# Kernel tuning notes

Hardware: AMD Instinct MI355X
Metric: run time of the kernel (lower is better)

## Reference

```python
import jax, jax.numpy as jnp
import numpy as np

D = 768      # d_model (BERT-base)
H = 8        # MatTransformer heads
DK = D // H  # 96
L = 4        # MatTransformer layers
FF = 1024    # MatTransformer hidden_size
NREL = 97    # num_relations
BAG = 8      # bag_len (docs per bag)
SEQ = 512    # seq_len
NB = 3       # bridge entities per doc
S = 2 + NB   # spans per doc: h, t, bridges
E = BAG * S  # total entities = 40
NEG = -1e30


def setup_inputs() -> dict:
    key = jax.random.key(0)
    ks = jax.random.split(key, 30)
    w = lambda k, shp: jax.random.normal(k, shp, jnp.float32) * 0.02
    inp = {
        "embedding": jax.random.normal(ks[0], (BAG, SEQ, D), jnp.float32),
        "spans": jnp.sort(jax.random.randint(ks[1], (BAG, S, 2), 0, SEQ, jnp.int32), axis=-1),
        # Codred pairwise-relation params (torch Linear stored as [in, out])
        "wu_w": w(ks[2], (D, D)), "wu_b": jnp.zeros((D,), jnp.float32),
        "wvv_w": w(ks[3], (D, D)), "wvv_b": jnp.zeros((D,), jnp.float32),
        "lnr_w": w(ks[4], (D, D)), "lnr_b": jnp.zeros((D,), jnp.float32),
        # MatTransformer params, stacked over layers
        "matt_wq": w(ks[5], (L, D, D)), "matt_bq": jnp.zeros((L, D), jnp.float32),
        "matt_wk": w(ks[6], (L, D, D)), "matt_bk": jnp.zeros((L, D), jnp.float32),
        "matt_wv": w(ks[7], (L, D, D)), "matt_bv": jnp.zeros((L, D), jnp.float32),
        "matt_wo": w(ks[8], (L, D, D)), "matt_bo": jnp.zeros((L, D), jnp.float32),
        "matt_w1": w(ks[9], (L, D, FF)), "matt_b1": jnp.zeros((L, FF), jnp.float32),
        "matt_w2": w(ks[10], (L, FF, D)), "matt_b2": jnp.zeros((L, D), jnp.float32),
        "matt_g1": jnp.ones((L, D), jnp.float32), "matt_be1": jnp.zeros((L, D), jnp.float32),
        "matt_g2": jnp.ones((L, D), jnp.float32), "matt_be2": jnp.zeros((L, D), jnp.float32),
        # relation predictor
        "pred_w": w(ks[11], (D, NREL)), "pred_b": jnp.zeros((NREL,), jnp.float32),
    }
    return inp


def _layernorm(x, g, b, eps=1e-5):
    m = jnp.mean(x, axis=-1, keepdims=True)
    v = jnp.var(x, axis=-1, keepdims=True)
    return (x - m) * jax.lax.rsqrt(v + eps) * g + b


def reference(embedding, spans, wu_w, wu_b, wvv_w, wvv_b, lnr_w, lnr_b,
              matt_wq, matt_bq, matt_wk, matt_bk, matt_wv, matt_bv, matt_wo, matt_bo,
              matt_w1, matt_b1, matt_w2, matt_b2, matt_g1, matt_be1, matt_g2, matt_be2,
              pred_w, pred_b):
    # --- entity span max-pool (gather + max over inclusive [start, end]) ---
    pos = jnp.arange(SEQ)
    span_mask = (pos[None, None, :] >= spans[..., 0:1]) & (pos[None, None, :] <= spans[..., 1:2])  # [BAG,S,SEQ]
    pooled = jnp.max(jnp.where(span_mask[..., None], embedding[:, None, :, :], NEG), axis=2)  # [BAG,S,D]
    htb = pooled.reshape(E, D)  # per-doc order: h, t, b1..bNB (matches htb_embs stacking)

    # --- pairwise relation matrix: relu(ln1(relu(u_i + v_j))) ---
    u = htb @ wu_w + wu_b                       # [E,D]
    v = htb @ wvv_w + wvv_b                     # [E,D]
    alpha = jax.nn.relu(u[:, None, :] + v[None, :, :])          # [E,E,D]
    rel = jax.nn.relu(alpha @ lnr_w + lnr_b)                    # [E,E,D]

    # --- MatTransformer: encoder over the E*E relation tokens (rel_mask all ones) ---
    T = E * E
    x = rel.reshape(T, D)
    scale = 1.0 / np.sqrt(DK).astype(np.float32)
    for l in range(L):
        q = (x @ matt_wq[l] + matt_bq[l]).reshape(T, H, DK)
        k = (x @ matt_wk[l] + matt_bk[l]).reshape(T, H, DK)
        vv = (x @ matt_wv[l] + matt_bv[l]).reshape(T, H, DK)
        scores = jnp.einsum('thd,shd->hts', q, k) * scale       # [H,T,T]
        attn = jax.nn.softmax(scores, axis=-1)
        o = jnp.einsum('hts,shd->thd', attn, vv).reshape(T, D)
        o = o @ matt_wo[l] + matt_bo[l]
        x = _layernorm(x + o, matt_g1[l], matt_be1[l])
        ff = jax.nn.relu(x @ matt_w1[l] + matt_b1[l]) @ matt_w2[l] + matt_b2[l]
        x = _layernorm(x + ff, matt_g2[l], matt_be2[l])
    rel_m = x.reshape(E, E, D)

    # --- gather (h, t) relation features, predict, bag max-pool over logits ---
    h_pos = jnp.arange(BAG) * S      # head entity index per doc
    t_pos = h_pos + 1                # tail entity index per doc
    ht_feat = rel_m[h_pos, t_pos]    # [BAG,D]
    ht_logits = ht_feat @ pred_w + pred_b          # [BAG,NREL]
    bag_logit = jnp.max(ht_logits, axis=0, keepdims=True)  # [1,NREL]
    return bag_logit
```

## Files before the change

### kernel.cpp

```cpp
#include <hip/hip_runtime.h>


#define D    768
#define H    8
#define DKD  96
#define LAY  4
#define FFD  1024
#define NREL 97
#define BAG  8
#define SPANS 5
#define E    40
#define TT   1600
#define SEQ  512
#define D3   2304
#define NS   3
#define QT   (TT / 64)

typedef __attribute__((ext_vector_type(8))) short bf16x8;
typedef __attribute__((ext_vector_type(4))) float f32x4;
typedef unsigned short ushort_t;
typedef unsigned int uint_t;

__device__ __forceinline__ ushort_t f2b(float x) {
    uint_t u = __builtin_bit_cast(uint_t, x);
    return (ushort_t)((u + 0x7fffu + ((u >> 16) & 1u)) >> 16);
}
__device__ __forceinline__ float b2f(ushort_t v) {
    return __builtin_bit_cast(float, (uint_t)v << 16);
}

__device__ __forceinline__ void gload16(const void* g, void* l) {
    __builtin_amdgcn_global_load_lds(
        (const __attribute__((address_space(1))) unsigned int*)g,
        (__attribute__((address_space(3))) unsigned int*)l, 16, 0, 0);
}

__device__ __forceinline__ float block_sum(float v, float* red) {
#pragma unroll
    for (int o = 32; o >= 1; o >>= 1) v += __shfl_xor(v, o);
    __syncthreads();
    if ((threadIdx.x & 63) == 0) red[threadIdx.x >> 6] = v;
    __syncthreads();
    return red[0] + red[1] + red[2] + red[3];
}

__global__ __launch_bounds__(256) void span_pool_p1(const float* __restrict__ emb,
        const int* __restrict__ spans, float* __restrict__ partial) {
    const int e = blockIdx.x, pg = blockIdx.y;
    const int bag = e / SPANS;
    const int st = spans[e * 2 + 0];
    const int en = spans[e * 2 + 1];
    const int p0 = max(st, pg * 64);
    const int p1 = min(en, pg * 64 + 63);
    const int tid = threadIdx.x;
    if (tid >= 192) return;
    float4 m = make_float4(-1e30f, -1e30f, -1e30f, -1e30f);
    for (int p = p0; p <= p1; ++p) {
        const float4 v = *(const float4*)(emb + ((size_t)bag * SEQ + p) * D + tid * 4);
        m.x = fmaxf(m.x, v.x); m.y = fmaxf(m.y, v.y);
        m.z = fmaxf(m.z, v.z); m.w = fmaxf(m.w, v.w);
    }
    *(float4*)(partial + ((size_t)e * 8 + pg) * D + tid * 4) = m;
}

__global__ __launch_bounds__(256) void span_pool_p2(const float* __restrict__ partial,
        ushort_t* __restrict__ htb) {
    const int e = blockIdx.x;
    const int tid = threadIdx.x;
    if (tid >= 192) return;
    float4 m = make_float4(-1e30f, -1e30f, -1e30f, -1e30f);
#pragma unroll
    for (int pg = 0; pg < 8; ++pg) {
        const float4 v = *(const float4*)(partial + ((size_t)e * 8 + pg) * D + tid * 4);
        m.x = fmaxf(m.x, v.x); m.y = fmaxf(m.y, v.y);
        m.z = fmaxf(m.z, v.z); m.w = fmaxf(m.w, v.w);
    }
    ushort4 o;
    o.x = f2b(m.x); o.y = f2b(m.y); o.z = f2b(m.z); o.w = f2b(m.w);
    *(ushort4*)(htb + (size_t)e * D + tid * 4) = o;
}

__global__ __launch_bounds__(256) void alpha_k(const float* __restrict__ uv,
        ushort_t* __restrict__ a) {
    const int ij = blockIdx.x;
    const int i = ij / E, j = ij % E;
    const int tid = threadIdx.x;
#pragma unroll
    for (int t2 = 0; t2 < 3; ++t2) {
        const int d = tid + t2 * 256;
        a[(size_t)ij * D + d] =
            f2b(fmaxf(uv[(size_t)i * 1536 + d] + uv[(size_t)j * 1536 + 768 + d], 0.f));
    }
}

__global__ __launch_bounds__(256) void transpose_up(const float* __restrict__ lnr,
        const float* __restrict__ wu, const float* __restrict__ wvv,
        ushort_t* __restrict__ lnrT, ushort_t* __restrict__ wuvT) {
    __shared__ float t[32][33];
    const int z = blockIdx.z;
    const float* src = (z == 0) ? lnr : (z == 1) ? wu : wvv;
    ushort_t* dst = (z == 0) ? lnrT : wuvT + (size_t)(z - 1) * D * D;
    const int n0 = blockIdx.x * 32, k0 = blockIdx.y * 32;
    const int tx = threadIdx.x & 31, ty = threadIdx.x >> 5;
#pragma unroll
    for (int i = 0; i < 4; ++i)
        t[ty + i * 8][tx] = src[(size_t)(k0 + ty + i * 8) * D + n0 + tx];
    __syncthreads();
#pragma unroll
    for (int i = 0; i < 4; ++i)
        dst[(size_t)(n0 + ty + i * 8) * D + k0 + tx] = f2b(t[tx][ty + i * 8]);
}

__global__ __launch_bounds__(256) void transpose_layer(const float* __restrict__ wq,
        const float* __restrict__ wk, const float* __restrict__ wv,
        const float* __restrict__ wo, const float* __restrict__ w1,
        const float* __restrict__ w2, int l, ushort_t* __restrict__ wT4,
        ushort_t* __restrict__ w1T, ushort_t* __restrict__ w2T) {
    __shared__ float t[32][33];
    const int z = blockIdx.z;
    const float* src; ushort_t* dst; int K, N;
    if (z < 4) {
        K = D; N = D;
        src = (z == 0 ? wq : z == 1 ? wk : z == 2 ? wv : wo) + (size_t)l * D * D;
        dst = wT4 + (size_t)z * D * D;
    } else if (z == 4) {
        K = D; N = FFD; src = w1 + (size_t)l * D * FFD; dst = w1T;
    } else {
        K = FFD; N = D; src = w2 + (size_t)l * FFD * D; dst = w2T;
    }
    const int n0 = blockIdx.x * 32, k0 = blockIdx.y * 32;
    if (n0 >= N || k0 >= K) return;
    const int tx = threadIdx.x & 31, ty = threadIdx.x >> 5;
#pragma unroll
    for (int i = 0; i < 4; ++i)
        t[ty + i * 8][tx] = src[(size_t)(k0 + ty + i * 8) * N + n0 + tx];
    __syncthreads();
#pragma unroll
    for (int i = 0; i < 4; ++i)
        dst[(size_t)(n0 + ty + i * 8) * K + k0 + tx] = f2b(t[tx][ty + i * 8]);
}

__global__ __launch_bounds__(256) void concat_bias(const float* __restrict__ bq,
        const float* __restrict__ bk, const float* __restrict__ bv,
        const float* __restrict__ bu, const float* __restrict__ bvv,
        float* __restrict__ bqkv, float* __restrict__ buv) {
    const int i = blockIdx.x * 256 + threadIdx.x;
    if (i < LAY * D3) {
        const int l = i / D3, j = i % D3;
        bqkv[i] = j < D ? bq[l * D + j] : j < 2 * D ? bk[l * D + j - D] : bv[l * D + j - 2 * D];
    }
    const int k = i - LAY * D3;
    if (k >= 0 && k < 2 * D) buv[k] = k < D ? bu[k] : bvv[k - D];
}

template<int RELU, int SCALEQ, int SPLITK, int HEADMAJ>
__global__ __launch_bounds__(256) void gemm_mfma(const ushort_t* __restrict__ A,
        const ushort_t* __restrict__ Bt, const float* __restrict__ bias,
        float* __restrict__ Cf, float* __restrict__ Cf1,
        ushort_t* __restrict__ Cb, int M, int N, int K) {
    __shared__ ushort_t As[2][128 * 32];
    __shared__ ushort_t Bs[2][64 * 32];
    const int tid = threadIdx.x;
    const int lane = tid & 63, w = tid >> 6;
    const int l15 = lane & 15, lg = lane >> 4;
    const int bm = blockIdx.y * 128, bn = blockIdx.x * 64;
    const int wm = (w >> 1) * 64, wn = (w & 1) * 32;
    const int trA0 = w * 32 + (lane >> 2);
    const int trA1 = trA0 + 16;
    const int trB  = w * 16 + (lane >> 2);
    const int sc   = (lane & 3) * 8;
    const size_t rowA0 = (size_t)min(bm + trA0, M - 1) * K;
    const size_t rowA1 = (size_t)min(bm + trA1, M - 1) * K;
    const size_t rowB  = (size_t)(bn + trB) * K;
    const int kbeg = SPLITK ? blockIdx.z * (K / 2) : 0;
    const int kend = SPLITK ? kbeg + K / 2 : K;

    f32x4 acc[4][2];
#pragma unroll
    for (int mi = 0; mi < 4; ++mi)
#pragma unroll
        for (int ni = 0; ni < 2; ++ni)
            acc[mi][ni] = (f32x4){0.f, 0.f, 0.f, 0.f};

    auto STAGE = [&](int buf, int k0) {
        gload16(A + rowA0 + k0 + sc, As[buf] + w * 1024);
        gload16(A + rowA1 + k0 + sc, As[buf] + w * 1024 + 512);
        gload16(Bt + rowB + k0 + sc, Bs[buf] + w * 512);
    };

    const int ntk = (kend - kbeg) / 32;
    STAGE(0, kbeg);
    __syncthreads();
    for (int t = 0; t < ntk; ++t) {
        const int buf = t & 1;
        if (t + 1 < ntk) STAGE(buf ^ 1, kbeg + (t + 1) * 32);
        bf16x8 af[4], bfr[2];
#pragma unroll
        for (int mi = 0; mi < 4; ++mi)
            af[mi] = *(const bf16x8*)&As[buf][(wm + mi * 16 + l15) * 32 + lg * 8];
#pragma unroll
        for (int ni = 0; ni < 2; ++ni)
            bfr[ni] = *(const bf16x8*)&Bs[buf][(wn + ni * 16 + l15) * 32 + lg * 8];
        __builtin_amdgcn_s_setprio(1);
#pragma unroll
        for (int mi = 0; mi < 4; ++mi)
#pragma unroll
            for (int ni = 0; ni < 2; ++ni)
                acc[mi][ni] = __builtin_amdgcn_mfma_f32_16x16x32_bf16(
                    af[mi], bfr[ni], acc[mi][ni], 0, 0, 0);
        __builtin_amdgcn_s_setprio(0);
        __syncthreads();
    }
    float* Cout = (SPLITK && blockIdx.z) ? Cf1 : Cf;
    const bool addb = !(SPLITK && blockIdx.z);
#pragma unroll
    for (int mi = 0; mi < 4; ++mi)
#pragma unroll
        for (int ni = 0; ni < 2; ++ni)
#pragma unroll
            for (int r = 0; r < 4; ++r) {
                const int row = bm + wm + mi * 16 + lg * 4 + r;
                if (row >= M) continue;
                const int col = bn + wn + ni * 16 + l15;
                float v = acc[mi][ni][r] + (addb ? bias[col] : 0.f);
                if (RELU) v = fmaxf(v, 0.f);
                if (SCALEQ) { if (col < D) v *= 0.10206207261596577f; }
                if (Cout) Cout[(size_t)row * N + col] = v;
                if (Cb) {
                    if (HEADMAJ) {
                        const int m = col / D;
                        const int rem = col - m * D;
                        const int hd = rem / DKD;
                        const int dd = rem - hd * DKD;
                        Cb[(((size_t)m * H + hd) * TT + row) * DKD + dd] = f2b(v);
                    } else {
                        Cb[(size_t)row * N + col] = f2b(v);
                    }
                }
            }
}

__global__ __launch_bounds__(256) void attn_part(const ushort_t* __restrict__ kvh,
        ushort_t* __restrict__ Opart, float* __restrict__ ml) {
    __shared__ ushort_t Ks[64][104];
    __shared__ ushort_t Vt[96][72];
    __shared__ ushort_t Ps[4][16][72];
    const int q0 = blockIdx.x * 64;
    const int h = blockIdx.y;
    const int cch = blockIdx.z;
    const int t_lo = (cch * QT) / NS;
    const int t_hi = ((cch + 1) * QT) / NS;
    const int tid = threadIdx.x;
    const int lane = tid & 63, w = tid >> 6;
    const int l15 = lane & 15, lg = lane >> 4;

    const ushort_t* Qb = kvh + (size_t)h * TT * DKD;
    const ushort_t* Kb = kvh + ((size_t)H + h) * TT * DKD;
    const ushort_t* Vb = kvh + ((size_t)2 * H + h) * TT * DKD;

    int r_[3], c_[3];
#pragma unroll
    for (int i = 0; i < 3; ++i) {
        const int ch = i * 256 + tid;
        r_[i] = ch / 12; c_[i] = (ch % 12) * 8;
    }
    bf16x8 qfrag[3];
#pragma unroll
    for (int ks = 0; ks < 3; ++ks)
        qfrag[ks] = *(const bf16x8*)(Qb + (size_t)(q0 + w * 16 + l15) * DKD
                                     + ks * 32 + lg * 8);
    uint4 kreg[3], vreg[3];
    {
        const int s0 = t_lo * 64;
#pragma unroll
        for (int i = 0; i < 3; ++i) {
            kreg[i] = *(const uint4*)(Kb + (size_t)(s0 + r_[i]) * DKD + c_[i]);
            vreg[i] = *(const uint4*)(Vb + (size_t)(s0 + r_[i]) * DKD + c_[i]);
        }
    }
    float m_run[4], l_run[4];
    f32x4 acc_o[6];
#pragma unroll
    for (int r = 0; r < 4; ++r) { m_run[r] = -1e30f; l_run[r] = 0.f; }
#pragma unroll
    for (int nt = 0; nt < 6; ++nt) acc_o[nt] = (f32x4){0.f, 0.f, 0.f, 0.f};

    for (int t = t_lo; t < t_hi; ++t) {
        __syncthreads();
#pragma unroll
        for (int i = 0; i < 3; ++i) {
            *(uint4*)&Ks[r_[i]][c_[i]] = kreg[i];
            const ushort_t* pv = (const ushort_t*)&vreg[i];
            const int kk = r_[i] ^ (((c_[i] >> 3) & 7) << 3);
#pragma unroll
            for (int j = 0; j < 8; ++j) Vt[c_[i] + j][kk] = pv[j];
        }
        __syncthreads();
        if (t + 1 < t_hi) {
            const int s0 = (t + 1) * 64;
#pragma unroll
            for (int i = 0; i < 3; ++i) {
                kreg[i] = *(const uint4*)(Kb + (size_t)(s0 + r_[i]) * DKD + c_[i]);
                vreg[i] = *(const uint4*)(Vb + (size_t)(s0 + r_[i]) * DKD + c_[i]);
            }
        }
        f32x4 accs[4];
#pragma unroll
        for (int ni = 0; ni < 4; ++ni) accs[ni] = (f32x4){0.f, 0.f, 0.f, 0.f};
        __builtin_amdgcn_s_setprio(1);
#pragma unroll
        for (int ks = 0; ks < 3; ++ks) {
#pragma unroll
            for (int ni = 0; ni < 4; ++ni) {
                const bf16x8 bk = *(const bf16x8*)&Ks[ni * 16 + l15][ks * 32 + lg * 8];
                accs[ni] = __builtin_amdgcn_mfma_f32_16x16x32_bf16(qfrag[ks], bk, accs[ni], 0, 0, 0);
            }
        }
        __builtin_amdgcn_s_setprio(0);
        float mx[4];
#pragma unroll
        for (int r = 0; r < 4; ++r) {
            mx[r] = fmaxf(fmaxf(accs[0][r], accs[1][r]), fmaxf(accs[2][r], accs[3][r]));
#pragma unroll
            for (int o = 1; o <= 8; o <<= 1) mx[r] = fmaxf(mx[r], __shfl_xor(mx[r], o));
        }
        const bool grow = (mx[0] > m_run[0] + 8.f) || (mx[1] > m_run[1] + 8.f) ||
                          (mx[2] > m_run[2] + 8.f) || (mx[3] > m_run[3] + 8.f);
        if (__any(grow)) {
#pragma unroll
            for (int r = 0; r < 4; ++r) {
                const float mnew = fmaxf(m_run[r], mx[r]);
                const float sf = __expf(m_run[r] - mnew);
                m_run[r] = mnew;
                l_run[r] *= sf;
#pragma unroll
                for (int nt = 0; nt < 6; ++nt) acc_o[nt][r] *= sf;
            }
        }
        float ps[4][4];
#pragma unroll
        for (int r = 0; r < 4; ++r) {
            float rs = 0.f;
#pragma unroll
            for (int ni = 0; ni < 4; ++ni) {
                ps[ni][r] = __expf(accs[ni][r] - m_run[r]);
                rs += ps[ni][r];
            }
#pragma unroll
            for (int o = 1; o <= 8; o <<= 1) rs += __shfl_xor(rs, o);
            l_run[r] += rs;
        }
#pragma unroll
        for (int ni = 0; ni < 4; ++ni)
#pragma unroll
            for (int r = 0; r < 4; ++r)
                Ps[w][lg * 4 + r][ni * 16 + l15] = f2b(ps[ni][r]);
        __builtin_amdgcn_s_setprio(1);
#pragma unroll
        for (int ks = 0; ks < 2; ++ks) {
            const bf16x8 ap = *(const bf16x8*)&Ps[w][l15][ks * 32 + lg * 8];
#pragma unroll
            for (int nt = 0; nt < 6; ++nt) {
                const int dim = nt * 16 + l15;
                const int kcol = (ks * 32 + lg * 8) ^ (((dim >> 3) & 7) << 3);
                const bf16x8 bv = *(const bf16x8*)&Vt[dim][kcol];
                acc_o[nt] = __builtin_amdgcn_mfma_f32_16x16x32_bf16(ap, bv, acc_o[nt], 0, 0, 0);
            }
        }
        __builtin_amdgcn_s_setprio(0);
    }
    __syncthreads();
    ushort_t* scr = &Ks[0][0] + w * (16 * 104);
#pragma unroll
    for (int nt = 0; nt < 6; ++nt)
#pragma unroll
        for (int r = 0; r < 4; ++r)
            scr[(lg * 4 + r) * 104 + nt * 16 + l15] = f2b(acc_o[nt][r]);
    const size_t obase = (((size_t)cch * H + h) * TT + q0 + w * 16) * DKD;
#pragma unroll
    for (int ch = 0; ch < 3; ++ch) {
        const int idx = ch * 64 + lane;
        const int row = idx / 12;
        const int c16 = (idx % 12) * 8;
        const uint4 v = *(const uint4*)&scr[row * 104 + c16];
        *(uint4*)(Opart + obase + (size_t)row * DKD + c16) = v;
    }
    if (l15 == 0) {
#pragma unroll
        for (int r = 0; r < 4; ++r) {
            const int row = q0 + w * 16 + lg * 4 + r;
            float2* mlp = (float2*)ml;
            mlp[((size_t)cch * H + h) * TT + row] = make_float2(m_run[r], l_run[r]);
        }
    }
}

__global__ __launch_bounds__(256) void attn_combine(const ushort_t* __restrict__ Opart,
        const float* __restrict__ ml, ushort_t* __restrict__ O) {
    const int lane = threadIdx.x & 63, w = threadIdx.x >> 6;
    const int row = blockIdx.x * 4 + w;
    const int hd = lane >> 3;
    const int co = (lane & 7) * 12;
    const float2* mlp = (const float2*)ml;
    float m[NS], l[NS], M = -1e30f;
#pragma unroll
    for (int c = 0; c < NS; ++c) {
        const float2 v = mlp[((size_t)c * H + hd) * TT + row];
        m[c] = v.x; l[c] = v.y; M = fmaxf(M, m[c]);
    }
    float e[NS], L = 0.f;
#pragma unroll
    for (int c = 0; c < NS; ++c) { e[c] = __expf(m[c] - M); L += l[c] * e[c]; }
    const float invL = 1.f / L;
    float o[12] = {};
#pragma unroll
    for (int c = 0; c < NS; ++c) {
        const ushort_t* p = Opart + (((size_t)c * H + hd) * TT + row) * DKD + co;
#pragma unroll
        for (int j = 0; j < 3; ++j) {
            const ushort4 v4 = *(const ushort4*)(p + j * 4);
            o[j * 4 + 0] += b2f(v4.x) * e[c];
            o[j * 4 + 1] += b2f(v4.y) * e[c];
            o[j * 4 + 2] += b2f(v4.z) * e[c];
            o[j * 4 + 3] += b2f(v4.w) * e[c];
        }
    }
    ushort_t* q = O + (size_t)row * D + hd * DKD + co;
#pragma unroll
    for (int j = 0; j < 3; ++j) {
        ushort4 u;
        u.x = f2b(o[j * 4 + 0] * invL); u.y = f2b(o[j * 4 + 1] * invL);
        u.z = f2b(o[j * 4 + 2] * invL); u.w = f2b(o[j * 4 + 3] * invL);
        *(ushort4*)(q + j * 4) = u;
    }
}

__global__ __launch_bounds__(256) void add_ln3(float* __restrict__ x,
        const float* __restrict__ y0, const float* __restrict__ y1,
        const float* __restrict__ g, const float* __restrict__ b,
        ushort_t* __restrict__ xb) {
    const int lane = threadIdx.x & 63, w = threadIdx.x >> 6;
    const int row = blockIdx.x * 4 + w;
    const size_t base = (size_t)row * D;
    float4 t[3];
    float s = 0.f, s2 = 0.f;
#pragma unroll
    for (int i = 0; i < 3; ++i) {
        const int c = lane * 4 + i * 256;
        const float4 xv = *(const float4*)(x + base + c);
        const float4 a0 = *(const float4*)(y0 + base + c);
        const float4 a1 = *(const float4*)(y1 + base + c);
        t[i].x = xv.x + a0.x + a1.x; t[i].y = xv.y + a0.y + a1.y;
        t[i].z = xv.z + a0.z + a1.z; t[i].w = xv.w + a0.w + a1.w;
        s += t[i].x + t[i].y + t[i].z + t[i].w;
        s2 += t[i].x * t[i].x + t[i].y * t[i].y + t[i].z * t[i].z + t[i].w * t[i].w;
    }
#pragma unroll
    for (int o = 32; o >= 1; o >>= 1) { s += __shfl_xor(s, o); s2 += __shfl_xor(s2, o); }
    const float mean = s * (1.f / 768.f);
    const float var = s2 * (1.f / 768.f) - mean * mean;
    const float inv = rsqrtf(var + 1e-5f);
#pragma unroll
    for (int i = 0; i < 3; ++i) {
        const int c = lane * 4 + i * 256;
        float4 o4;
        o4.x = (t[i].x - mean) * inv * g[c + 0] + b[c + 0];
        o4.y = (t[i].y - mean) * inv * g[c + 1] + b[c + 1];
        o4.z = (t[i].z - mean) * inv * g[c + 2] + b[c + 2];
        o4.w = (t[i].w - mean) * inv * g[c + 3] + b[c + 3];
        *(float4*)(x + base + c) = o4;
        ushort4 u;
        u.x = f2b(o4.x); u.y = f2b(o4.y); u.z = f2b(o4.z); u.w = f2b(o4.w);
        *(ushort4*)(xb + base + c) = u;
    }
}

__global__ __launch_bounds__(256) void predict_k(const float* __restrict__ x,
        const float* __restrict__ pw, const float* __restrict__ pb,
        float* __restrict__ out) {
    __shared__ float red[4];
    const int r = blockIdx.x;
    const int tid = threadIdx.x;
    float best = -1e30f;
    for (int bag = 0; bag < BAG; ++bag) {
        const int row = (bag * SPANS) * E + (bag * SPANS + 1);
        const float* f = x + (size_t)row * D;
        float acc = 0.f;
        for (int d = tid; d < D; d += 256) acc += f[d] * pw[(size_t)d * NREL + r];
        best = fmaxf(best, block_sum(acc, red));
    }
    if (tid == 0) out[r] = best + pb[r];
}

extern "C" void kernel_launch(void* const* d_in, const int* in_sizes, int n_in,
                              void* d_out, int out_size, void* d_ws, size_t ws_size,
                              hipStream_t stream) {
    const float* emb  = (const float*)d_in[0];
    const int*  spans = (const int*)d_in[1];
    const float* wu_w = (const float*)d_in[2];  const float* wu_b = (const float*)d_in[3];
    const float* wvv_w= (const float*)d_in[4];  const float* wvv_b= (const float*)d_in[5];
    const float* lnr_w= (const float*)d_in[6];  const float* lnr_b= (const float*)d_in[7];
    const float* wq = (const float*)d_in[8];    const float* bq = (const float*)d_in[9];
    const float* wk = (const float*)d_in[10];   const float* bk = (const float*)d_in[11];
    const float* wv = (const float*)d_in[12];   const float* bv = (const float*)d_in[13];
    const float* wo = (const float*)d_in[14];   const float* bo = (const float*)d_in[15];
    const float* w1 = (const float*)d_in[16];   const float* b1 = (const float*)d_in[17];
    const float* w2 = (const float*)d_in[18];   const float* b2 = (const float*)d_in[19];
    const float* g1 = (const float*)d_in[20];   const float* be1= (const float*)d_in[21];
    const float* g2 = (const float*)d_in[22];   const float* be2= (const float*)d_in[23];
    const float* pw = (const float*)d_in[24];   const float* pb = (const float*)d_in[25];

    char* cur = (char*)d_ws;
    auto alloc = [&](size_t bytes) { char* p = cur; cur += (bytes + 255) & ~(size_t)255; return p; };
    ushort_t* htb  = (ushort_t*)alloc(E * D * 2);
    float*    uvb  = (float*)alloc((size_t)E * 1536 * 4);
    float*    part = (float*)alloc((size_t)E * 8 * D * 4);
    float*    x    = (float*)alloc((size_t)TT * D * 4);
    ushort_t* xb   = (ushort_t*)alloc((size_t)TT * D * 2);
    ushort_t* kvh  = (ushort_t*)alloc((size_t)3 * H * TT * DKD * 2);
    ushort_t* ob   = (ushort_t*)alloc((size_t)TT * D * 2);
    float*    tb   = (float*)alloc((size_t)TT * D * 4);
    ushort_t* fb   = (ushort_t*)alloc((size_t)TT * FFD * 2);
    ushort_t* wT4  = (ushort_t*)alloc((size_t)4 * D * D * 2);
    ushort_t* w1T  = (ushort_t*)alloc((size_t)D * FFD * 2);
    ushort_t* w2T  = (ushort_t*)alloc((size_t)FFD * D * 2);
    float*    bqkv = (float*)alloc((size_t)LAY * D3 * 4);
    float*    buv  = (float*)alloc((size_t)2 * D * 4);
    ushort_t* Opart = (ushort_t*)tb;
    float*    ml    = part;
    ushort_t* wuvT  = wT4;
    ushort_t* lnrT  = w1T;
    float*    tb1   = (float*)kvh;

    const int DD = D * D;

    span_pool_p1<<<dim3(E, 8), 256, 0, stream>>>(emb, spans, part);
    span_pool_p2<<<E, 256, 0, stream>>>(part, htb);
    transpose_up<<<dim3(24, 24, 3), 256, 0, stream>>>(lnr_w, wu_w, wvv_w, lnrT, wuvT);
    concat_bias<<<(LAY * D3 + 2 * D + 255) / 256, 256, 0, stream>>>(bq, bk, bv, wu_b, wvv_b, bqkv, buv);
    gemm_mfma<0, 0, 0, 0><<<dim3(1536 / 64, 1), 256, 0, stream>>>(
        htb, wuvT, buv, uvb, nullptr, nullptr, E, 1536, D);
    alpha_k<<<TT, 256, 0, stream>>>(uvb, ob);
    gemm_mfma<1, 0, 0, 0><<<dim3(D / 64, (TT + 127) / 128), 256, 0, stream>>>(
        ob, lnrT, lnr_b, x, nullptr, xb, TT, D, D);

    for (int l = 0; l < LAY; ++l) {
        transpose_layer<<<dim3(32, 32, 6), 256, 0, stream>>>(wq, wk, wv, wo, w1, w2, l, wT4, w1T, w2T);
        gemm_mfma<0, 1, 0, 1><<<dim3(D3 / 64, (TT + 127) / 128), 256, 0, stream>>>(
            xb, wT4, bqkv + l * D3, nullptr, nullptr, kvh, TT, D3, D);
        attn_part<<<dim3(QT, H, NS), 256, 0, stream>>>(kvh, Opart, ml);
        attn_combine<<<TT / 4, 256, 0, stream>>>(Opart, ml, ob);
        gemm_mfma<0, 0, 1, 0><<<dim3(D / 64, (TT + 127) / 128, 2), 256, 0, stream>>>(
            ob, wT4 + 3 * DD, bo + l * D, tb, tb1, nullptr, TT, D, D);
        add_ln3<<<TT / 4, 256, 0, stream>>>(x, tb, tb1, g1 + l * D, be1 + l * D, xb);
        gemm_mfma<1, 0, 0, 0><<<dim3(FFD / 64, (TT + 127) / 128), 256, 0, stream>>>(
            xb, w1T, b1 + l * FFD, nullptr, nullptr, fb, TT, FFD, D);
        gemm_mfma<0, 0, 1, 0><<<dim3(D / 64, (TT + 127) / 128, 2), 256, 0, stream>>>(
            fb, w2T, b2 + l * D, tb, tb1, nullptr, TT, D, FFD);
        add_ln3<<<TT / 4, 256, 0, stream>>>(x, tb, tb1, g2 + l * D, be2 + l * D, xb);
    }

    predict_k<<<NREL, 256, 0, stream>>>(x, pw, pb, (float*)d_out);
    (void)in_sizes; (void)n_in; (void)out_size; (void)ws_size;
}
```

Baseline: 593.7 us.

## Process two query tiles per attention block to reuse K/V tiles

Each attn_part block now handles two 64-row query tiles (qx and qx+13) against each loaded K/V tile, halving the grid in the x dimension from 25 to 13. This is meant to halve the number of K/V global loads and LDS transposes per query row and give each wave twice the MFMA work per sync. The cost is higher register pressure from doubled accumulators and softmax state, fewer blocks (13x8x3 = 312) and so possibly lower occupancy. There is also wasted MFMA work in the last block, where tile B is clamped and skipped.

```diff
diff --git a/kernel.cpp b/kernel.cpp
--- a/kernel.cpp
+++ b/kernel.cpp
@@ -15,6 +15,7 @@
 #define D3   2304
 #define NS   3
 #define QT   (TT / 64)
+#define QX   13
 
 typedef __attribute__((ext_vector_type(8))) short bf16x8;
 typedef __attribute__((ext_vector_type(4))) float f32x4;
@@ -244,8 +245,12 @@
         ushort_t* __restrict__ Opart, float* __restrict__ ml) {
     __shared__ ushort_t Ks[64][104];
     __shared__ ushort_t Vt[96][72];
-    __shared__ ushort_t Ps[4][16][72];
-    const int q0 = blockIdx.x * 64;
+    __shared__ ushort_t PsA[4][16][72];
+    __shared__ ushort_t PsB[4][16][72];
+    const int qx = blockIdx.x;
+    const int q0a = qx * 64;
+    const int q0b = (qx + QX) * 64;
+    const bool hasB = (qx + QX) < QT;
     const int h = blockIdx.y;
     const int cch = blockIdx.z;
     const int t_lo = (cch * QT) / NS;
@@ -264,11 +269,12 @@
         const int ch = i * 256 + tid;
         r_[i] = ch / 12; c_[i] = (ch % 12) * 8;
     }
-    bf16x8 qfrag[3];
-#pragma unroll
-    for (int ks = 0; ks < 3; ++ks)
-        qfrag[ks] = *(const bf16x8*)(Qb + (size_t)(q0 + w * 16 + l15) * DKD
-                                     + ks * 32 + lg * 8);
+    bf16x8 qfA[3], qfB[3];
+#pragma unroll
+    for (int ks = 0; ks < 3; ++ks) {
+        qfA[ks] = *(const bf16x8*)(Qb + (size_t)(q0a + w * 16 + l15) * DKD + ks * 32 + lg * 8);
+        qfB[ks] = *(const bf16x8*)(Qb + (size_t)(min(q0b, TT - 64) + w * 16 + l15) * DKD + ks * 32 + lg * 8);
+    }
     uint4 kreg[3], vreg[3];
     {
         const int s0 = t_lo * 64;
@@ -278,12 +284,12 @@
             vreg[i] = *(const uint4*)(Vb + (size_t)(s0 + r_[i]) * DKD + c_[i]);
         }
     }
-    float m_run[4], l_run[4];
-    f32x4 acc_o[6];
-#pragma unroll
-    for (int r = 0; r < 4; ++r) { m_run[r] = -1e30f; l_run[r] = 0.f; }
-#pragma unroll
-    for (int nt = 0; nt < 6; ++nt) acc_o[nt] = (f32x4){0.f, 0.f, 0.f, 0.f};
+    float mA[4], lA[4], mB[4], lB[4];
+    f32x4 oA[6], oB[6];
+#pragma unroll
+    for (int r = 0; r < 4; ++r) { mA[r] = -1e30f; lA[r] = 0.f; mB[r] = -1e30f; lB[r] = 0.f; }
+#pragma unroll
+    for (int nt = 0; nt < 6; ++nt) { oA[nt] = (f32x4){0.f,0.f,0.f,0.f}; oB[nt] = (f32x4){0.f,0.f,0.f,0.f}; }
 
     for (int t = t_lo; t < t_hi; ++t) {
         __syncthreads();
@@ -304,93 +310,154 @@
                 vreg[i] = *(const uint4*)(Vb + (size_t)(s0 + r_[i]) * DKD + c_[i]);
             }
         }
-        f32x4 accs[4];
-#pragma unroll
-        for (int ni = 0; ni < 4; ++ni) accs[ni] = (f32x4){0.f, 0.f, 0.f, 0.f};
+        f32x4 aA[4], aB[4];
+#pragma unroll
+        for (int ni = 0; ni < 4; ++ni) { aA[ni] = (f32x4){0.f,0.f,0.f,0.f}; aB[ni] = (f32x4){0.f,0.f,0.f,0.f}; }
         __builtin_amdgcn_s_setprio(1);
 #pragma unroll
-        for (int ks = 0; ks < 3; ++ks) {
+        for (int ks = 0; ks < 3; ++ks)
 #pragma unroll
             for (int ni = 0; ni < 4; ++ni) {
                 const bf16x8 bk = *(const bf16x8*)&Ks[ni * 16 + l15][ks * 32 + lg * 8];
-                accs[ni] = __builtin_amdgcn_mfma_f32_16x16x32_bf16(qfrag[ks], bk, accs[ni], 0, 0, 0);
-            }
-        }
+                aA[ni] = __builtin_amdgcn_mfma_f32_16x16x32_bf16(qfA[ks], bk, aA[ni], 0, 0, 0);
+                aB[ni] = __builtin_amdgcn_mfma_f32_16x16x32_bf16(qfB[ks], bk, aB[ni], 0, 0, 0);
+            }
         __builtin_amdgcn_s_setprio(0);
-        float mx[4];
-#pragma unroll
-        for (int r = 0; r < 4; ++r) {
-            mx[r] = fmaxf(fmaxf(accs[0][r], accs[1][r]), fmaxf(accs[2][r], accs[3][r]));
-#pragma unroll
-            for (int o = 1; o <= 8; o <<= 1) mx[r] = fmaxf(mx[r], __shfl_xor(mx[r], o));
-        }
-        const bool grow = (mx[0] > m_run[0] + 8.f) || (mx[1] > m_run[1] + 8.f) ||
-                          (mx[2] > m_run[2] + 8.f) || (mx[3] > m_run[3] + 8.f);
-        if (__any(grow)) {
+        {
+            float mx[4];
 #pragma unroll
             for (int r = 0; r < 4; ++r) {
-                const float mnew = fmaxf(m_run[r], mx[r]);
-                const float sf = __expf(m_run[r] - mnew);
-                m_run[r] = mnew;
-                l_run[r] *= sf;
-#pragma unroll
-                for (int nt = 0; nt < 6; ++nt) acc_o[nt][r] *= sf;
-            }
-        }
-        float ps[4][4];
-#pragma unroll
-        for (int r = 0; r < 4; ++r) {
-            float rs = 0.f;
-#pragma unroll
-            for (int ni = 0; ni < 4; ++ni) {
-                ps[ni][r] = __expf(accs[ni][r] - m_run[r]);
-                rs += ps[ni][r];
-            }
-#pragma unroll
-            for (int o = 1; o <= 8; o <<= 1) rs += __shfl_xor(rs, o);
-            l_run[r] += rs;
-        }
-#pragma unroll
-        for (int ni = 0; ni < 4; ++ni)
-#pragma unroll
-            for (int r = 0; r < 4; ++r)
-                Ps[w][lg * 4 + r][ni * 16 + l15] = f2b(ps[ni][r]);
+                mx[r] = fmaxf(fmaxf(aA[0][r], aA[1][r]), fmaxf(aA[2][r], aA[3][r]));
+#pragma unroll
+                for (int o = 1; o <= 8; o <<= 1) mx[r] = fmaxf(mx[r], __shfl_xor(mx[r], o));
+            }
+            const bool grow = (mx[0] > mA[0] + 8.f) || (mx[1] > mA[1] + 8.f) ||
+                              (mx[2] > mA[2] + 8.f) || (mx[3] > mA[3] + 8.f);
+            if (__any(grow)) {
+#pragma unroll
+                for (int r = 0; r < 4; ++r) {
+                    const float mn = fmaxf(mA[r], mx[r]);
+                    const float sf = __expf(mA[r] - mn);
+                    mA[r] = mn; lA[r] *= sf;
+#pragma unroll
+                    for (int nt = 0; nt < 6; ++nt) oA[nt][r] *= sf;
+                }
+            }
+            float ps[4][4];
+#pragma unroll
+            for (int r = 0; r < 4; ++r) {
+                float rs = 0.f;
+#pragma unroll
+                for (int ni = 0; ni < 4; ++ni) { ps[ni][r] = __expf(aA[ni][r] - mA[r]); rs += ps[ni][r]; }
+#pragma unroll
+                for (int o = 1; o <= 8; o <<= 1) rs += __shfl_xor(rs, o);
+                lA[r] += rs;
+            }
+#pragma unroll
+            for (int ni = 0; ni < 4; ++ni)
+#pragma unroll
+                for (int r = 0; r < 4; ++r)
+                    PsA[w][lg * 4 + r][ni * 16 + l15] = f2b(ps[ni][r]);
+        }
+        if (hasB) {
+            float mx[4];
+#pragma unroll
+            for (int r = 0; r < 4; ++r) {
+                mx[r] = fmaxf(fmaxf(aB[0][r], aB[1][r]), fmaxf(aB[2][r], aB[3][r]));
+#pragma unroll
+                for (int o = 1; o <= 8; o <<= 1) mx[r] = fmaxf(mx[r], __shfl_xor(mx[r], o));
+            }
+            const bool grow = (mx[0] > mB[0] + 8.f) || (mx[1] > mB[1] + 8.f) ||
+                              (mx[2] > mB[2] + 8.f) || (mx[3] > mB[3] + 8.f);
+            if (__any(grow)) {
+#pragma unroll
+                for (int r = 0; r < 4; ++r) {
+                    const float mn = fmaxf(mB[r], mx[r]);
+                    const float sf = __expf(mB[r] - mn);
+                    mB[r] = mn; lB[r] *= sf;
+#pragma unroll
+                    for (int nt = 0; nt < 6; ++nt) oB[nt][r] *= sf;
+                }
+            }
+            float ps[4][4];
+#pragma unroll
+            for (int r = 0; r < 4; ++r) {
+                float rs = 0.f;
+#pragma unroll
+                for (int ni = 0; ni < 4; ++ni) { ps[ni][r] = __expf(aB[ni][r] - mB[r]); rs += ps[ni][r]; }
+#pragma unroll
+                for (int o = 1; o <= 8; o <<= 1) rs += __shfl_xor(rs, o);
+                lB[r] += rs;
+            }
+#pragma unroll
+            for (int ni = 0; ni < 4; ++ni)
+#pragma unroll
+                for (int r = 0; r < 4; ++r)
+                    PsB[w][lg * 4 + r][ni * 16 + l15] = f2b(ps[ni][r]);
+        }
         __builtin_amdgcn_s_setprio(1);
 #pragma unroll
         for (int ks = 0; ks < 2; ++ks) {
-            const bf16x8 ap = *(const bf16x8*)&Ps[w][l15][ks * 32 + lg * 8];
+            const bf16x8 apA = *(const bf16x8*)&PsA[w][l15][ks * 32 + lg * 8];
+            const bf16x8 apB = *(const bf16x8*)&PsB[w][l15][ks * 32 + lg * 8];
 #pragma unroll
             for (int nt = 0; nt < 6; ++nt) {
                 const int dim = nt * 16 + l15;
                 const int kcol = (ks * 32 + lg * 8) ^ (((dim >> 3) & 7) << 3);
                 const bf16x8 bv = *(const bf16x8*)&Vt[dim][kcol];
-                acc_o[nt] = __builtin_amdgcn_mfma_f32_16x16x32_bf16(ap, bv, acc_o[nt], 0, 0, 0);
+                oA[nt] = __builtin_amdgcn_mfma_f32_16x16x32_bf16(apA, bv, oA[nt], 0, 0, 0);
+                oB[nt] = __builtin_amdgcn_mfma_f32_16x16x32_bf16(apB, bv, oB[nt], 0, 0, 0);
             }
         }
         __builtin_amdgcn_s_setprio(0);
     }
+    ushort_t* scr = &Ks[0][0] + w * (16 * 104);
     __syncthreads();
-    ushort_t* scr = &Ks[0][0] + w * (16 * 104);
 #pragma unroll
     for (int nt = 0; nt < 6; ++nt)
 #pragma unroll
         for (int r = 0; r < 4; ++r)
-            scr[(lg * 4 + r) * 104 + nt * 16 + l15] = f2b(acc_o[nt][r]);
-    const size_t obase = (((size_t)cch * H + h) * TT + q0 + w * 16) * DKD;
-#pragma unroll
-    for (int ch = 0; ch < 3; ++ch) {
-        const int idx = ch * 64 + lane;
-        const int row = idx / 12;
-        const int c16 = (idx % 12) * 8;
-        const uint4 v = *(const uint4*)&scr[row * 104 + c16];
-        *(uint4*)(Opart + obase + (size_t)row * DKD + c16) = v;
+            scr[(lg * 4 + r) * 104 + nt * 16 + l15] = f2b(oA[nt][r]);
+    {
+        const size_t obase = (((size_t)cch * H + h) * TT + q0a + w * 16) * DKD;
+#pragma unroll
+        for (int ch = 0; ch < 3; ++ch) {
+            const int idx = ch * 64 + lane;
+            const int row = idx / 12;
+            const int c16 = (idx % 12) * 8;
+            const uint4 v = *(const uint4*)&scr[row * 104 + c16];
+            *(uint4*)(Opart + obase + (size_t)row * DKD + c16) = v;
+        }
     }
     if (l15 == 0) {
 #pragma unroll
         for (int r = 0; r < 4; ++r) {
-            const int row = q0 + w * 16 + lg * 4 + r;
-            float2* mlp = (float2*)ml;
-            mlp[((size_t)cch * H + h) * TT + row] = make_float2(m_run[r], l_run[r]);
+            const int row = q0a + w * 16 + lg * 4 + r;
+            ((float2*)ml)[((size_t)cch * H + h) * TT + row] = make_float2(mA[r], lA[r]);
+        }
+    }
+    if (hasB) {
+        __syncthreads();
+#pragma unroll
+        for (int nt = 0; nt < 6; ++nt)
+#pragma unroll
+            for (int r = 0; r < 4; ++r)
+                scr[(lg * 4 + r) * 104 + nt * 16 + l15] = f2b(oB[nt][r]);
+        const size_t obase = (((size_t)cch * H + h) * TT + q0b + w * 16) * DKD;
+#pragma unroll
+        for (int ch = 0; ch < 3; ++ch) {
+            const int idx = ch * 64 + lane;
+            const int row = idx / 12;
+            const int c16 = (idx % 12) * 8;
+            const uint4 v = *(const uint4*)&scr[row * 104 + c16];
+            *(uint4*)(Opart + obase + (size_t)row * DKD + c16) = v;
+        }
+        if (l15 == 0) {
+#pragma unroll
+            for (int r = 0; r < 4; ++r) {
+                const int row = q0b + w * 16 + lg * 4 + r;
+                ((float2*)ml)[((size_t)cch * H + h) * TT + row] = make_float2(mB[r], lB[r]);
+            }
         }
     }
 }
@@ -548,7 +615,7 @@
         transpose_layer<<<dim3(32, 32, 6), 256, 0, stream>>>(wq, wk, wv, wo, w1, w2, l, wT4, w1T, w2T);
         gemm_mfma<0, 1, 0, 1><<<dim3(D3 / 64, (TT + 127) / 128), 256, 0, stream>>>(
             xb, wT4, bqkv + l * D3, nullptr, nullptr, kvh, TT, D3, D);
-        attn_part<<<dim3(QT, H, NS), 256, 0, stream>>>(kvh, Opart, ml);
+        attn_part<<<dim3(QX, H, NS), 256, 0, stream>>>(kvh, Opart, ml);
         attn_combine<<<TT / 4, 256, 0, stream>>>(Opart, ml, ob);
         gemm_mfma<0, 0, 1, 0><<<dim3(D / 64, (TT + 127) / 128, 2), 256, 0, stream>>>(
             ob, wT4 + 3 * DD, bo + l * D, tb, tb1, nullptr, TT, D, D);
```

After: 608.2 us. 2.5% more time.
